# Kernel tuning notes

Hardware: AMD Instinct MI355X
Metric: run time of the kernel (lower is better)

Reference implementation:

```python
import jax, jax.numpy as jnp
import numpy as np
from jax import lax

B, CIN, IMG = 32, 3, 128   # batch, image channels, image size
D, K = 256, 512            # codebook dim, codebook size


def _conv(x, w, stride, pad):
    # PyTorch Conv2d (bias=False), NCHW / OIHW
    return lax.conv_general_dilated(x, w, (stride, stride), ((pad, pad), (pad, pad)),
                                    dimension_numbers=('NCHW', 'OIHW', 'NCHW'))


def _deconv(x, w, b):
    # PyTorch ConvTranspose2d(k=4, s=2, p=1): lhs_dilation=2, pad=k-1-p=2, flipped kernel,
    # weight layout (in, out, kh, kw) -> 'IOHW'
    y = lax.conv_general_dilated(x, jnp.flip(w, (2, 3)), (1, 1), ((2, 2), (2, 2)),
                                 lhs_dilation=(2, 2),
                                 dimension_numbers=('NCHW', 'IOHW', 'NCHW'))
    return y + b[None, :, None, None]


def _res(x, w1, w2):
    # Faithful to the source ResidualBlock: relu1 output is DISCARDED (conv1 applied to x)
    out = _conv(x, w1, 1, 1)      # 3x3, pad 1
    out = jax.nn.relu(out)
    out = _conv(out, w2, 1, 0)    # 1x1, pad 0
    return out + x


def setup_inputs() -> dict:
    key = jax.random.key(0)
    ks = jax.random.split(key, 20)
    s = 0.05
    inp = {
        'x': jax.random.uniform(ks[0], (B, CIN, IMG, IMG), jnp.float32),
        # codebook, init uniform(-1/K, 1/K) as in init_weights
        'embed_w': jax.random.uniform(ks[1], (K, D), jnp.float32, -1.0 / K, 1.0 / K),
        # encoder
        'e_w1': jax.random.normal(ks[2], (D, CIN, 4, 4), jnp.float32) * s,
        'e_w2': jax.random.normal(ks[3], (D, D, 4, 4), jnp.float32) * s,
        'e_r1a': jax.random.normal(ks[4], (D, D, 3, 3), jnp.float32) * s,
        'e_r1b': jax.random.normal(ks[5], (D, D, 1, 1), jnp.float32) * s,
        'e_r2a': jax.random.normal(ks[6], (D, D, 3, 3), jnp.float32) * s,
        'e_r2b': jax.random.normal(ks[7], (D, D, 1, 1), jnp.float32) * s,
        # decoder
        'd_r1a': jax.random.normal(ks[8], (D, D, 3, 3), jnp.float32) * s,
        'd_r1b': jax.random.normal(ks[9], (D, D, 1, 1), jnp.float32) * s,
        'd_r2a': jax.random.normal(ks[10], (D, D, 3, 3), jnp.float32) * s,
        'd_r2b': jax.random.normal(ks[11], (D, D, 1, 1), jnp.float32) * s,
        'dt1_w': jax.random.normal(ks[12], (D, D, 4, 4), jnp.float32) * s,  # (in,out,kh,kw)
        'dt1_b': jnp.zeros((D,), jnp.float32),
        'dt2_w': jax.random.normal(ks[13], (D, CIN, 4, 4), jnp.float32) * s,
        'dt2_b': jnp.zeros((CIN,), jnp.float32),
    }
    return inp


def reference(x, embed_w, e_w1, e_w2, e_r1a, e_r1b, e_r2a, e_r2b,
              d_r1a, d_r1b, d_r2a, d_r2b, dt1_w, dt1_b, dt2_w, dt2_b):
    # ---- encoder (BN layers exist but are never called in the source forward) ----
    h = jax.nn.relu(_conv(x, e_w1, 2, 1))          # (B,D,64,64)
    h = jax.nn.relu(_conv(h, e_w2, 2, 1))          # (B,D,32,32)
    h = _res(h, e_r1a, e_r1b)
    z_e = _res(h, e_r2a, e_r2b)                    # (B,D,H,W)

    # ---- vector quantisation ----
    ze = jnp.transpose(z_e, (0, 2, 3, 1))          # (B,H,W,D)
    # squared L2 distances via expansion (same argmin/values as the broadcast diff tensor)
    d2 = (jnp.sum(ze * ze, -1, keepdims=True)      # (B,H,W,1)
          - 2.0 * jnp.einsum('bhwd,kd->bhwk', ze, embed_w)
          + jnp.sum(embed_w * embed_w, -1))        # (B,H,W,K)
    dist = jnp.sqrt(jnp.maximum(d2, 0.0))          # torch.norm(p=2) before min
    idx = jnp.argmin(dist, axis=-1)                # (B,H,W)
    z_q = embed_w[idx]                             # (B,H,W,D) gather

    # losses: source averages over an extra duplicated K axis, identical to mean over B,H,W
    sg = lax.stop_gradient
    loss1 = jnp.mean(jnp.sum((ze - sg(z_q)) ** 2, -1))   # grads -> encoder
    loss2 = jnp.mean(jnp.sum((sg(ze) - z_q) ** 2, -1))   # grads -> codebook

    # ---- decoder (takes z_q; BN layers never called; relu after deconv1 only) ----
    dq = jnp.transpose(z_q, (0, 3, 1, 2))          # (B,D,H,W)
    dq = _res(dq, d_r1a, d_r1b)
    dq = _res(dq, d_r2a, d_r2b)
    dq = jax.nn.relu(_deconv(dq, dt1_w, dt1_b))    # (B,D,64,64)
    recon = jax.nn.sigmoid(_deconv(dq, dt2_w, dt2_b))  # (B,3,128,128)
    return recon, loss1, loss2
```

## Files before the change

kernel.cpp:

```cpp
#include <hip/hip_runtime.h>


typedef __attribute__((ext_vector_type(8))) short bf16x8;
typedef __attribute__((ext_vector_type(4))) float f32x4;
#define MFMA_B16(a, b, c) __builtin_amdgcn_mfma_f32_16x16x32_bf16(a, b, c, 0, 0, 0)

__device__ inline unsigned short f2b(float f) {
    unsigned int u = __float_as_uint(f);
    unsigned int r = u + 0x7fffu + ((u >> 16) & 1u);
    return (unsigned short)(r >> 16);
}
__device__ inline float b2f(unsigned short u) {
    return __uint_as_float(((unsigned int)u) << 16);
}

struct PermfArgs {
    const float* src[10];
    int kw[10];
    int so[10], si[10], sh[10], sw[10];
    int cum[11];
};

__global__ void prep_all_k(PermfArgs a, unsigned short* __restrict__ dst,
                           const float* __restrict__ dt2_w, unsigned short* __restrict__ wg,
                           const float* __restrict__ embed, unsigned short* __restrict__ embF,
                           const float* __restrict__ e_w1, unsigned short* __restrict__ wgc,
                           float* __restrict__ nrm, float* __restrict__ lacc)
{
    int blkid = blockIdx.x;
    int tid = threadIdx.x;
    if (blkid < 18432) {
        int gid = blkid * 256 + tid;
        if (gid >= a.cum[10]) return;
        int seg = 0;
        while (seg < 9 && gid >= a.cum[seg + 1]) ++seg;
        int l = gid - a.cum[seg];
        int q = l & 31;
        int n = (l >> 5) & 255;
        int rest = l >> 13;
        int cch = rest & 7;
        int khkw = rest >> 3;
        int kh = khkw / a.kw[seg], kw = khkw % a.kw[seg];
        int ci = cch * 32 + q;
        dst[gid] = f2b(a.src[seg][n * a.so[seg] + ci * a.si[seg] + kh * a.sh[seg] + kw * a.sw[seg]]);
        return;
    }
    int blk = blkid - 18432;
    if (blk < 48) {
        int idx = blk * 256 + tid;
        int q = idx & 31;
        int n = (idx >> 5) % 48;
        int cch = idx / (48 * 32);
        int ci = cch * 32 + q;
        int oc = n % 3, khkw = n / 3;
        int kh = khkw >> 2, kw = khkw & 3;
        wg[idx] = f2b(dt2_w[ci * 48 + oc * 16 + kh * 4 + kw]);
    } else if (blk < 560) {
        int idx = (blk - 48) * 256 + tid;
        int q = idx & 31;
        int n = (idx >> 5) & 511;
        int cch = idx >> 14;
        embF[idx] = f2b(embed[n * 256 + cch * 32 + q]);
    } else if (blk < 624) {
        int idx = (blk - 560) * 256 + tid;
        int q = idx & 31;
        int n = (idx >> 5) & 255;
        int kt = idx >> 13;
        int k = kt * 32 + q;
        float v = 0.f;
        if (k < 48) {
            int ci = k >> 4, kh = (k >> 2) & 3, kwv = k & 3;
            v = e_w1[n * 48 + ci * 16 + kh * 4 + kwv];
        }
        wgc[idx] = f2b(v);
    } else if (blk < 752) {
        int row = (blk - 624) * 4 + (tid >> 6);
        int lane = tid & 63;
        float s = 0.f;
        #pragma unroll
        for (int c = 0; c < 256; c += 64) {
            float v = embed[row * 256 + c + lane];
            s += v * v;
        }
        #pragma unroll
        for (int off = 1; off < 64; off <<= 1) s += __shfl_xor(s, off);
        if (lane == 0) nrm[row] = s;
    } else {
        if (tid == 0) lacc[0] = 0.f;
    }
}

__global__ void __launch_bounds__(256, 4)
conv1m_k(const float* __restrict__ x, const unsigned short* __restrict__ wgc,
         unsigned short* __restrict__ out)
{
    int bh = blockIdx.x;
    int b = bh >> 6, oh = bh & 63;
    int tid = threadIdx.x;
    int lane = tid & 63, wv = tid >> 6;
    int m = lane & 15, quad = lane >> 4;
    __shared__ float xrow[3][4][130];
    __shared__ __align__(16) unsigned short imc[64 * 72];
    for (int s = tid; s < 1560; s += 256) {
        int col = s % 130;
        int t = s / 130;
        int r = t & 3;
        int c = t >> 2;
        int ih = 2 * oh - 1 + r, iw = col - 1;
        float v = 0.f;
        if ((unsigned)ih < 128u && (unsigned)iw < 128u)
            v = x[(((b * 3 + c) << 7) + ih) * 128 + iw];
        xrow[c][r][col] = v;
    }
    __syncthreads();
    for (int s = tid; s < 4096; s += 256) {
        int px = s >> 6, k = s & 63;
        float v = 0.f;
        if (k < 48) {
            int ci = k >> 4, kh = (k >> 2) & 3, kw = k & 3;
            v = xrow[ci][kh][2 * px + kw];
        }
        imc[px * 72 + k] = f2b(v);
    }
    __syncthreads();
    f32x4 acc[16];
    f32x4 z = {0.f, 0.f, 0.f, 0.f};
    #pragma unroll
    for (int i = 0; i < 16; ++i) acc[i] = z;
    bf16x8 a0 = *(const bf16x8*)&imc[((wv << 4) + m) * 72 + (quad << 3)];
    bf16x8 a1 = *(const bf16x8*)&imc[((wv << 4) + m) * 72 + 32 + (quad << 3)];
    #pragma unroll
    for (int nt = 0; nt < 16; ++nt) {
        bf16x8 b0 = *(const bf16x8*)&wgc[(nt * 16 + m) * 32 + (quad << 3)];
        bf16x8 b1 = *(const bf16x8*)&wgc[(256 + nt * 16 + m) * 32 + (quad << 3)];
        acc[nt] = MFMA_B16(a0, b0, acc[nt]);
        acc[nt] = MFMA_B16(a1, b1, acc[nt]);
    }
    #pragma unroll
    for (int nt = 0; nt < 16; ++nt)
        #pragma unroll
        for (int r = 0; r < 4; ++r) {
            int px = (wv << 4) + quad * 4 + r;
            out[(((bh << 6) + px) << 8) + nt * 16 + (lane & 15)] = f2b(fmaxf(acc[nt][r], 0.f));
        }
}

__global__ void __launch_bounds__(256, 3)
mconv2_k(const unsigned short* __restrict__ in, const unsigned short* __restrict__ wf,
         unsigned short* __restrict__ out)
{
    int blk = blockIdx.x;
    int bb = blk >> 4, j = blk & 15;
    int lane = threadIdx.x & 63;
    int n0 = (threadIdx.x >> 6) << 6;
    int m = lane & 15, quad = lane >> 4;
    __shared__ __align__(16) unsigned short win[2 * 66 * 132];
    f32x4 acc[2][2][4];
    f32x4 z = {0.f, 0.f, 0.f, 0.f};
    #pragma unroll
    for (int a = 0; a < 2; ++a)
        #pragma unroll
        for (int i = 0; i < 2; ++i)
            #pragma unroll
            for (int t = 0; t < 4; ++t) acc[a][i][t] = z;

    for (int c0 = 0; c0 < 256; c0 += 128) {
        for (int kh = 0; kh < 4; ++kh) {
            __syncthreads();
            for (int s = threadIdx.x; s < 2 * 66 * 16; s += 256) {
                int c16 = s & 15;
                int t2 = s >> 4;
                int col = t2 % 66;
                int rr = t2 / 66;
                int ih = 4 * j - 1 + kh + 2 * rr, iw = col - 1;
                int4 v = make_int4(0, 0, 0, 0);
                if ((unsigned)ih < 64u && (unsigned)iw < 64u)
                    v = *(const int4*)&in[((((bb << 6) + ih) << 6) + iw) * 256 + c0 + (c16 << 3)];
                int cs = (col >> 1) + (col & 1) * 33;
                *(int4*)&win[(rr * 66 + cs) * 132 + (c16 << 3)] = v;
            }
            __syncthreads();
            #pragma unroll
            for (int kw = 0; kw < 4; ++kw) {
                int csoff = (kw >> 1) + (kw & 1) * 33;
                #pragma unroll
                for (int cch = 0; cch < 4; ++cch) {
                    bf16x8 a00 = *(const bf16x8*)&win[(m + csoff) * 132 + (cch << 5) + (quad << 3)];
                    bf16x8 a01 = *(const bf16x8*)&win[(m + 16 + csoff) * 132 + (cch << 5) + (quad << 3)];
                    bf16x8 a10 = *(const bf16x8*)&win[(66 + m + csoff) * 132 + (cch << 5) + (quad << 3)];
                    bf16x8 a11 = *(const bf16x8*)&win[(66 + m + 16 + csoff) * 132 + (cch << 5) + (quad << 3)];
                    int cg = (c0 >> 5) + cch;
                    int wbase = ((((kh << 2) + kw) * 8 + cg) * 256 + n0 + m) * 32 + (quad << 3);
                    bf16x8 b0 = *(const bf16x8*)&wf[wbase];
                    bf16x8 b1 = *(const bf16x8*)&wf[wbase + 16 * 32];
                    bf16x8 b2 = *(const bf16x8*)&wf[wbase + 32 * 32];
                    bf16x8 b3 = *(const bf16x8*)&wf[wbase + 48 * 32];
                    acc[0][0][0] = MFMA_B16(a00, b0, acc[0][0][0]);
                    acc[0][0][1] = MFMA_B16(a00, b1, acc[0][0][1]);
                    acc[0][0][2] = MFMA_B16(a00, b2, acc[0][0][2]);
                    acc[0][0][3] = MFMA_B16(a00, b3, acc[0][0][3]);
                    acc[0][1][0] = MFMA_B16(a01, b0, acc[0][1][0]);
                    acc[0][1][1] = MFMA_B16(a01, b1, acc[0][1][1]);
                    acc[0][1][2] = MFMA_B16(a01, b2, acc[0][1][2]);
                    acc[0][1][3] = MFMA_B16(a01, b3, acc[0][1][3]);
                    acc[1][0][0] = MFMA_B16(a10, b0, acc[1][0][0]);
                    acc[1][0][1] = MFMA_B16(a10, b1, acc[1][0][1]);
                    acc[1][0][2] = MFMA_B16(a10, b2, acc[1][0][2]);
                    acc[1][0][3] = MFMA_B16(a10, b3, acc[1][0][3]);
                    acc[1][1][0] = MFMA_B16(a11, b0, acc[1][1][0]);
                    acc[1][1][1] = MFMA_B16(a11, b1, acc[1][1][1]);
                    acc[1][1][2] = MFMA_B16(a11, b2, acc[1][1][2]);
                    acc[1][1][3] = MFMA_B16(a11, b3, acc[1][1][3]);
                }
            }
        }
    }
    #pragma unroll
    for (int row = 0; row < 2; ++row) {
        int oh = 2 * j + row;
        #pragma unroll
        for (int mt = 0; mt < 2; ++mt)
            #pragma unroll
            for (int nt = 0; nt < 4; ++nt)
                #pragma unroll
                for (int r = 0; r < 4; ++r) {
                    int px = mt * 16 + quad * 4 + r;
                    int col = n0 + nt * 16 + m;
                    out[((((bb << 5) + oh) << 5) + px) * 256 + col] = f2b(fmaxf(acc[row][mt][nt][r], 0.f));
                }
    }
}

__global__ void __launch_bounds__(256, 4)
mres_k(const unsigned short* __restrict__ in, const unsigned short* __restrict__ wf3,
       const unsigned short* __restrict__ wf1, const unsigned short* __restrict__ res,
       unsigned short* __restrict__ outb, float* __restrict__ outf, int f32out)
{
    int blk = blockIdx.x;
    int bb = blk >> 4, j = blk & 15;
    int lane = threadIdx.x & 63;
    int n0 = (threadIdx.x >> 6) << 6;
    int m = lane & 15, quad = lane >> 4;
    __shared__ __align__(16) unsigned short win[4 * 34 * 132];
    f32x4 acc[2][2][4];
    f32x4 z = {0.f, 0.f, 0.f, 0.f};
    #pragma unroll
    for (int a = 0; a < 2; ++a)
        #pragma unroll
        for (int i = 0; i < 2; ++i)
            #pragma unroll
            for (int t = 0; t < 4; ++t) acc[a][i][t] = z;

    for (int c0 = 0; c0 < 256; c0 += 128) {
        __syncthreads();
        for (int s = threadIdx.x; s < 4 * 34 * 16; s += 256) {
            int c16 = s & 15;
            int t2 = s >> 4;
            int col = t2 % 34;
            int rr = t2 / 34;
            int ih = 2 * j - 1 + rr, iw = col - 1;
            int4 v = make_int4(0, 0, 0, 0);
            if ((unsigned)ih < 32u && (unsigned)iw < 32u)
                v = *(const int4*)&in[((((bb << 5) + ih) << 5) + iw) * 256 + c0 + (c16 << 3)];
            *(int4*)&win[(rr * 34 + col) * 132 + (c16 << 3)] = v;
        }
        __syncthreads();
        for (int kh = 0; kh < 3; ++kh) {
            #pragma unroll
            for (int kw = 0; kw < 3; ++kw) {
                #pragma unroll
                for (int cch = 0; cch < 4; ++cch) {
                    const unsigned short* ba = &win[(kh * 34 + m + kw) * 132 + (cch << 5) + (quad << 3)];
                    bf16x8 a00 = *(const bf16x8*)ba;
                    bf16x8 a01 = *(const bf16x8*)(ba + 16 * 132);
                    bf16x8 a10 = *(const bf16x8*)(ba + 34 * 132);
                    bf16x8 a11 = *(const bf16x8*)(ba + 50 * 132);
                    int cg = (c0 >> 5) + cch;
                    int wbase = (((kh * 3 + kw) * 8 + cg) * 256 + n0 + m) * 32 + (quad << 3);
                    bf16x8 b0 = *(const bf16x8*)&wf3[wbase];
                    bf16x8 b1 = *(const bf16x8*)&wf3[wbase + 16 * 32];
                    bf16x8 b2 = *(const bf16x8*)&wf3[wbase + 32 * 32];
                    bf16x8 b3 = *(const bf16x8*)&wf3[wbase + 48 * 32];
                    acc[0][0][0] = MFMA_B16(a00, b0, acc[0][0][0]);
                    acc[0][0][1] = MFMA_B16(a00, b1, acc[0][0][1]);
                    acc[0][0][2] = MFMA_B16(a00, b2, acc[0][0][2]);
                    acc[0][0][3] = MFMA_B16(a00, b3, acc[0][0][3]);
                    acc[0][1][0] = MFMA_B16(a01, b0, acc[0][1][0]);
                    acc[0][1][1] = MFMA_B16(a01, b1, acc[0][1][1]);
                    acc[0][1][2] = MFMA_B16(a01, b2, acc[0][1][2]);
                    acc[0][1][3] = MFMA_B16(a01, b3, acc[0][1][3]);
                    acc[1][0][0] = MFMA_B16(a10, b0, acc[1][0][0]);
                    acc[1][0][1] = MFMA_B16(a10, b1, acc[1][0][1]);
                    acc[1][0][2] = MFMA_B16(a10, b2, acc[1][0][2]);
                    acc[1][0][3] = MFMA_B16(a10, b3, acc[1][0][3]);
                    acc[1][1][0] = MFMA_B16(a11, b0, acc[1][1][0]);
                    acc[1][1][1] = MFMA_B16(a11, b1, acc[1][1][1]);
                    acc[1][1][2] = MFMA_B16(a11, b2, acc[1][1][2]);
                    acc[1][1][3] = MFMA_B16(a11, b3, acc[1][1][3]);
                }
            }
        }
    }

    __syncthreads();
    unsigned short* mid = win;
    #pragma unroll
    for (int row = 0; row < 2; ++row)
        #pragma unroll
        for (int mt = 0; mt < 2; ++mt)
            #pragma unroll
            for (int nt = 0; nt < 4; ++nt)
                #pragma unroll
                for (int r = 0; r < 4; ++r) {
                    int px = row * 32 + mt * 16 + quad * 4 + r;
                    int col = n0 + nt * 16 + m;
                    mid[px * 264 + col] = f2b(fmaxf(acc[row][mt][nt][r], 0.f));
                }
    __syncthreads();

    f32x4 acc2[4][4];
    #pragma unroll
    for (int i = 0; i < 4; ++i)
        #pragma unroll
        for (int t = 0; t < 4; ++t) acc2[i][t] = z;
    #pragma unroll
    for (int cch = 0; cch < 8; ++cch) {
        bf16x8 a0 = *(const bf16x8*)&mid[m * 264 + (cch << 5) + (quad << 3)];
        bf16x8 a1 = *(const bf16x8*)&mid[(m + 16) * 264 + (cch << 5) + (quad << 3)];
        bf16x8 a2 = *(const bf16x8*)&mid[(m + 32) * 264 + (cch << 5) + (quad << 3)];
        bf16x8 a3 = *(const bf16x8*)&mid[(m + 48) * 264 + (cch << 5) + (quad << 3)];
        int wbase = (cch * 256 + n0 + m) * 32 + (quad << 3);
        bf16x8 b0 = *(const bf16x8*)&wf1[wbase];
        bf16x8 b1 = *(const bf16x8*)&wf1[wbase + 16 * 32];
        bf16x8 b2 = *(const bf16x8*)&wf1[wbase + 32 * 32];
        bf16x8 b3 = *(const bf16x8*)&wf1[wbase + 48 * 32];
        acc2[0][0] = MFMA_B16(a0, b0, acc2[0][0]);
        acc2[0][1] = MFMA_B16(a0, b1, acc2[0][1]);
        acc2[0][2] = MFMA_B16(a0, b2, acc2[0][2]);
        acc2[0][3] = MFMA_B16(a0, b3, acc2[0][3]);
        acc2[1][0] = MFMA_B16(a1, b0, acc2[1][0]);
        acc2[1][1] = MFMA_B16(a1, b1, acc2[1][1]);
        acc2[1][2] = MFMA_B16(a1, b2, acc2[1][2]);
        acc2[1][3] = MFMA_B16(a1, b3, acc2[1][3]);
        acc2[2][0] = MFMA_B16(a2, b0, acc2[2][0]);
        acc2[2][1] = MFMA_B16(a2, b1, acc2[2][1]);
        acc2[2][2] = MFMA_B16(a2, b2, acc2[2][2]);
        acc2[2][3] = MFMA_B16(a2, b3, acc2[2][3]);
        acc2[3][0] = MFMA_B16(a3, b0, acc2[3][0]);
        acc2[3][1] = MFMA_B16(a3, b1, acc2[3][1]);
        acc2[3][2] = MFMA_B16(a3, b2, acc2[3][2]);
        acc2[3][3] = MFMA_B16(a3, b3, acc2[3][3]);
    }
    int rowbase = blk << 14;
    #pragma unroll
    for (int mt = 0; mt < 4; ++mt)
        #pragma unroll
        for (int nt = 0; nt < 4; ++nt)
            #pragma unroll
            for (int r = 0; r < 4; ++r) {
                int px = mt * 16 + quad * 4 + r;
                int col = n0 + nt * 16 + m;
                int idx = rowbase + (px << 8) + col;
                float v = acc2[mt][nt][r] + b2f(res[idx]);
                outb[idx] = f2b(v);
                if (f32out) outf[idx] = v;
            }
}

__global__ void __launch_bounds__(256, 4)
mdeconv1_k(const unsigned short* __restrict__ in, const unsigned short* __restrict__ wf,
           const float* __restrict__ bias, unsigned short* __restrict__ out)
{
    int blk = blockIdx.x;
    int bb = blk >> 5;
    int rem = blk & 31;
    int pp = rem >> 4;
    int i = rem & 15;
    int oy_a = pp + 4 * i;
    int p = (oy_a + 1) & 1;
    int r0a = (oy_a + 1 - p) >> 1;
    int rbase = r0a - 1;
    int lane = threadIdx.x & 63;
    int n0 = (threadIdx.x >> 6) << 6;
    int m = lane & 15, quad = lane >> 4;
    __shared__ __align__(16) unsigned short win[2 * 34 * 264];

    auto stage_row = [&](int slot, int r) {
        int ih = rbase + r;
        for (int s = threadIdx.x; s < 34 * 32; s += 256) {
            int c8 = s & 31;
            int col = s >> 5;
            int iw = col - 1;
            int4 v = make_int4(0, 0, 0, 0);
            if ((unsigned)ih < 32u && (unsigned)iw < 32u)
                v = *(const int4*)&in[((((bb << 5) + ih) << 5) + iw) * 256 + (c8 << 3)];
            *(int4*)&win[(slot * 34 + col) * 264 + (c8 << 3)] = v;
        }
    };

    for (int par = 0; par < 2; ++par) {
        f32x4 acc[2][2][4];
        f32x4 z = {0.f, 0.f, 0.f, 0.f};
        #pragma unroll
        for (int a = 0; a < 2; ++a)
            #pragma unroll
            for (int i2 = 0; i2 < 2; ++i2)
                #pragma unroll
                for (int t = 0; t < 4; ++t) acc[a][i2][t] = z;

        __syncthreads();
        stage_row(0, 0);
        if (par == 0) stage_row(1, 1);
        __syncthreads();
        #pragma unroll
        for (int ph = 0; ph < 2; ++ph) {
            int t = 1 - ph;
            int kh = p + 2 * t;
            int slotA = ph;
            int slotB = 1 - ph;
            if (ph == 1) {
                __syncthreads();
                stage_row(0, 2);
                __syncthreads();
            }
            #pragma unroll
            for (int u = 0; u < 2; ++u) {
                int kw = (1 - par) + 2 * u;
                int ixoff = par - u + 1;
                #pragma unroll
                for (int cch = 0; cch < 8; ++cch) {
                    const unsigned short* baA = &win[(slotA * 34 + m + ixoff) * 264 + (cch << 5) + (quad << 3)];
                    const unsigned short* baB = &win[(slotB * 34 + m + ixoff) * 264 + (cch << 5) + (quad << 3)];
                    bf16x8 a00 = *(const bf16x8*)baA;
                    bf16x8 a01 = *(const bf16x8*)(baA + 16 * 264);
                    bf16x8 a10 = *(const bf16x8*)baB;
                    bf16x8 a11 = *(const bf16x8*)(baB + 16 * 264);
                    int wbase = ((((kh << 2) + kw) * 8 + cch) * 256 + n0 + m) * 32 + (quad << 3);
                    bf16x8 b0 = *(const bf16x8*)&wf[wbase];
                    bf16x8 b1 = *(const bf16x8*)&wf[wbase + 16 * 32];
                    bf16x8 b2 = *(const bf16x8*)&wf[wbase + 32 * 32];
                    bf16x8 b3 = *(const bf16x8*)&wf[wbase + 48 * 32];
                    acc[0][0][0] = MFMA_B16(a00, b0, acc[0][0][0]);
                    acc[0][0][1] = MFMA_B16(a00, b1, acc[0][0][1]);
                    acc[0][0][2] = MFMA_B16(a00, b2, acc[0][0][2]);
                    acc[0][0][3] = MFMA_B16(a00, b3, acc[0][0][3]);
                    acc[0][1][0] = MFMA_B16(a01, b0, acc[0][1][0]);
                    acc[0][1][1] = MFMA_B16(a01, b1, acc[0][1][1]);
                    acc[0][1][2] = MFMA_B16(a01, b2, acc[0][1][2]);
                    acc[0][1][3] = MFMA_B16(a01, b3, acc[0][1][3]);
                    acc[1][0][0] = MFMA_B16(a10, b0, acc[1][0][0]);
                    acc[1][0][1] = MFMA_B16(a10, b1, acc[1][0][1]);
                    acc[1][0][2] = MFMA_B16(a10, b2, acc[1][0][2]);
                    acc[1][0][3] = MFMA_B16(a10, b3, acc[1][0][3]);
                    acc[1][1][0] = MFMA_B16(a11, b0, acc[1][1][0]);
                    acc[1][1][1] = MFMA_B16(a11, b1, acc[1][1][1]);
                    acc[1][1][2] = MFMA_B16(a11, b2, acc[1][1][2]);
                    acc[1][1][3] = MFMA_B16(a11, b3, acc[1][1][3]);
                }
            }
        }
        #pragma unroll
        for (int row = 0; row < 2; ++row) {
            int oy = oy_a + 2 * row;
            #pragma unroll
            for (int mt = 0; mt < 2; ++mt)
                #pragma unroll
                for (int nt = 0; nt < 4; ++nt) {
                    int col = n0 + nt * 16 + m;
                    float bs = bias[col];
                    #pragma unroll
                    for (int r = 0; r < 4; ++r) {
                        int ox = 2 * (mt * 16 + quad * 4 + r) + par;
                        float v = fmaxf(acc[row][mt][nt][r] + bs, 0.f);
                        out[((((bb << 6) + oy) << 6) + ox) * 256 + col] = f2b(v);
                    }
                }
        }
    }
}

__global__ void __launch_bounds__(256, 2)
vqm_k(const unsigned short* __restrict__ zeb, const float* __restrict__ zef,
      const unsigned short* __restrict__ embF, const float* __restrict__ embed,
      const float* __restrict__ nrm, unsigned short* __restrict__ zq,
      float* __restrict__ lacc)
{
    int bh = blockIdx.x;
    int tid = threadIdx.x;
    int lane = tid & 63;
    int wv = tid >> 6;
    int m = lane & 15, quad = lane >> 4;
    __shared__ __align__(16) unsigned short win[32 * 264];
    __shared__ float bvv[4][32];
    __shared__ int   bii[4][32];
    __shared__ int   bidx[32];
    int rowbase = bh << 13;
    for (int s = tid; s < 32 * 32; s += 256) {
        int c8 = s & 31, px = s >> 5;
        *(int4*)&win[px * 264 + (c8 << 3)] = *(const int4*)&zeb[rowbase + (px << 8) + (c8 << 3)];
    }
    __syncthreads();

    f32x4 acc[2][8];
    f32x4 z = {0.f, 0.f, 0.f, 0.f};
    #pragma unroll
    for (int i = 0; i < 2; ++i)
        #pragma unroll
        for (int j = 0; j < 8; ++j) acc[i][j] = z;

    #pragma unroll
    for (int cch = 0; cch < 8; ++cch) {
        bf16x8 a0 = *(const bf16x8*)&win[m * 264 + (cch << 5) + (quad << 3)];
        bf16x8 a1 = *(const bf16x8*)&win[(m + 16) * 264 + (cch << 5) + (quad << 3)];
        #pragma unroll
        for (int nt = 0; nt < 8; ++nt) {
            bf16x8 b = *(const bf16x8*)&embF[((cch << 9) + (wv << 7) + (nt << 4) + m) * 32 + (quad << 3)];
            acc[0][nt] = MFMA_B16(a0, b, acc[0][nt]);
            acc[1][nt] = MFMA_B16(a1, b, acc[1][nt]);
        }
    }

    float nv[8];
    #pragma unroll
    for (int nt = 0; nt < 8; ++nt) nv[nt] = nrm[(wv << 7) + (nt << 4) + m];

    #pragma unroll
    for (int mt = 0; mt < 2; ++mt)
        #pragma unroll
        for (int r = 0; r < 4; ++r) {
            float bv = 1e30f;
            int bi = 0x7fffffff;
            #pragma unroll
            for (int nt = 0; nt < 8; ++nt) {
                float d = nv[nt] - 2.f * acc[mt][nt][r];
                int n = (wv << 7) + (nt << 4) + m;
                if (d < bv || (d == bv && n < bi)) { bv = d; bi = n; }
            }
            #pragma unroll
            for (int off = 1; off < 16; off <<= 1) {
                float ov = __shfl_xor(bv, off);
                int oi = __shfl_xor(bi, off);
                if (ov < bv || (ov == bv && oi < bi)) { bv = ov; bi = oi; }
            }
            if (m == 0) {
                int px = mt * 16 + quad * 4 + r;
                bvv[wv][px] = bv;
                bii[wv][px] = bi;
            }
        }
    __syncthreads();
    if (tid < 32) {
        float bv = bvv[0][tid];
        int bi = bii[0][tid];
        #pragma unroll
        for (int w2 = 1; w2 < 4; ++w2) {
            float ov = bvv[w2][tid];
            int oi = bii[w2][tid];
            if (ov < bv || (ov == bv && oi < bi)) { bv = ov; bi = oi; }
        }
        bidx[tid] = bi;
    }
    __syncthreads();

    float lsum = 0.f;
    #pragma unroll
    for (int j = 0; j < 8; ++j) {
        int px = (wv << 3) + j;
        int bi = bidx[px];
        int pix = (bh << 5) + px;
        const float4 e = *(const float4*)&embed[bi * 256 + (lane << 2)];
        const float4 zv = *(const float4*)&zef[(pix << 8) + (lane << 2)];
        ushort4 eq;
        eq.x = f2b(e.x); eq.y = f2b(e.y); eq.z = f2b(e.z); eq.w = f2b(e.w);
        *(ushort4*)&zq[(pix << 8) + (lane << 2)] = eq;
        float dx = zv.x - e.x, dy = zv.y - e.y, dz = zv.z - e.z, dw = zv.w - e.w;
        lsum += dx * dx + dy * dy + dz * dz + dw * dw;
    }
    #pragma unroll
    for (int off = 1; off < 64; off <<= 1) lsum += __shfl_xor(lsum, off);
    if (lane == 0) atomicAdd(lacc, lsum);
}

__global__ void __launch_bounds__(256, 4)
mdec2a_k(const unsigned short* __restrict__ in, const unsigned short* __restrict__ wg,
         float* __restrict__ Y)
{
    int tid = threadIdx.x;
    int lane = tid & 63;
    int wv = tid >> 6;
    int m = lane & 15, quad = lane >> 4;
    __shared__ __align__(16) unsigned short win[64 * 264];
    int pxbase = blockIdx.x << 6;
    for (int s = tid; s < 64 * 32; s += 256) {
        int c8 = s & 31, px = s >> 5;
        *(int4*)&win[px * 264 + (c8 << 3)] = *(const int4*)&in[((pxbase + px) << 8) + (c8 << 3)];
    }
    __syncthreads();
    f32x4 acc[3];
    f32x4 z = {0.f, 0.f, 0.f, 0.f};
    acc[0] = z; acc[1] = z; acc[2] = z;
    #pragma unroll
    for (int cch = 0; cch < 8; ++cch) {
        bf16x8 a = *(const bf16x8*)&win[((wv << 4) + m) * 264 + (cch << 5) + (quad << 3)];
        #pragma unroll
        for (int nt = 0; nt < 3; ++nt) {
            bf16x8 b = *(const bf16x8*)&wg[(cch * 48 + nt * 16 + m) * 32 + (quad << 3)];
            acc[nt] = MFMA_B16(a, b, acc[nt]);
        }
    }
    #pragma unroll
    for (int nt = 0; nt < 3; ++nt)
        #pragma unroll
        for (int r = 0; r < 4; ++r) {
            int px = pxbase + (wv << 4) + quad * 4 + r;
            Y[px * 48 + nt * 16 + m] = acc[nt][r];
        }
}

__global__ void dec2b_k(const float* __restrict__ Y, const float* __restrict__ bias,
                        const float* __restrict__ lacc, float* __restrict__ out)
{
    if (blockIdx.x == 0 && threadIdx.x == 0) {
        float mloss = lacc[0] * (1.0f / 32768.0f);
        out[1572864] = mloss;
        out[1572865] = mloss;
    }
    int idx = blockIdx.x * 256 + threadIdx.x;
    int b = idx >> 14;
    int rem = idx & 16383;
    int oy = rem >> 7;
    int ox = rem & 127;
    int p = (oy + 1) & 1;
    int q = (ox + 1) & 1;
    float acc0 = bias[0], acc1 = bias[1], acc2 = bias[2];
    #pragma unroll
    for (int t = 0; t < 2; ++t) {
        int kh = p + 2 * t;
        int ih = (oy + 1 - kh) >> 1;
        if ((unsigned)ih >= 64u) continue;
        #pragma unroll
        for (int u = 0; u < 2; ++u) {
            int kw = q + 2 * u;
            int iw = (ox + 1 - kw) >> 1;
            if ((unsigned)iw >= 64u) continue;
            int base = ((((b << 6) + ih) << 6) + iw) * 48 + ((kh << 2) + kw) * 3;
            acc0 += Y[base];
            acc1 += Y[base + 1];
            acc2 += Y[base + 2];
        }
    }
    int obase = (b * 3 << 14) + (oy << 7) + ox;
    out[obase]           = 1.f / (1.f + expf(-acc0));
    out[obase + 16384]   = 1.f / (1.f + expf(-acc1));
    out[obase + 32768]   = 1.f / (1.f + expf(-acc2));
}

extern "C" void kernel_launch(void* const* d_in, const int* in_sizes, int n_in,
                              void* d_out, int out_size, void* d_ws, size_t ws_size,
                              hipStream_t stream)
{
    (void)in_sizes; (void)n_in; (void)out_size; (void)ws_size;
    const float* x      = (const float*)d_in[0];
    const float* embed  = (const float*)d_in[1];
    const float* e_w1   = (const float*)d_in[2];
    const float* e_w2   = (const float*)d_in[3];
    const float* e_r1a  = (const float*)d_in[4];
    const float* e_r1b  = (const float*)d_in[5];
    const float* e_r2a  = (const float*)d_in[6];
    const float* e_r2b  = (const float*)d_in[7];
    const float* d_r1a  = (const float*)d_in[8];
    const float* d_r1b  = (const float*)d_in[9];
    const float* d_r2a  = (const float*)d_in[10];
    const float* d_r2b  = (const float*)d_in[11];
    const float* dt1_w  = (const float*)d_in[12];
    const float* dt1_b  = (const float*)d_in[13];
    const float* dt2_w  = (const float*)d_in[14];
    const float* dt2_b  = (const float*)d_in[15];
    float* outp = (float*)d_out;

    char* base = (char*)d_ws;
    size_t off = 0;
    auto alloc = [&](size_t bytes) { char* p = base + off; off += (bytes + 255) & ~size_t(255); return p; };
    unsigned short* A0b = (unsigned short*)alloc(67108864);
    float*          A1f = (float*)alloc(33554432);
    unsigned short* L0  = (unsigned short*)alloc(16777216);
    unsigned short* L1  = (unsigned short*)alloc(16777216);
    unsigned short* Wf  = (unsigned short*)alloc(9437184);
    unsigned short* Wg  = (unsigned short*)alloc(24576);
    unsigned short* EmbF = (unsigned short*)alloc(262144);
    unsigned short* WgC = (unsigned short*)alloc(32768);
    float* Nrm  = (float*)alloc(2048);
    float* Lacc = (float*)alloc(64);
    float* Y = A1f;

    unsigned short* Wf_ew2  = Wf;
    unsigned short* Wf_er1a = Wf + 1048576;
    unsigned short* Wf_er1b = Wf + 1638400;
    unsigned short* Wf_er2a = Wf + 1703936;
    unsigned short* Wf_er2b = Wf + 2293760;
    unsigned short* Wf_dr1a = Wf + 2359296;
    unsigned short* Wf_dr1b = Wf + 2949120;
    unsigned short* Wf_dr2a = Wf + 3014656;
    unsigned short* Wf_dr2b = Wf + 3604480;
    unsigned short* Wf_dt1  = Wf + 3670016;

    PermfArgs pa;
    const float* srcs[10] = {e_w2, e_r1a, e_r1b, e_r2a, e_r2b, d_r1a, d_r1b, d_r2a, d_r2b, dt1_w};
    int kws[10] = {4, 3, 1, 3, 1, 3, 1, 3, 1, 4};
    int sos[10] = {4096, 2304, 256, 2304, 256, 2304, 256, 2304, 256, 16};
    int sis[10] = {16, 9, 1, 9, 1, 9, 1, 9, 1, 4096};
    int shs[10] = {4, 3, 0, 3, 0, 3, 0, 3, 0, 4};
    int sws[10] = {1, 1, 0, 1, 0, 1, 0, 1, 0, 1};
    int cums[11] = {0, 1048576, 1638400, 1703936, 2293760, 2359296,
                    2949120, 3014656, 3604480, 3670016, 4718592};
    for (int k = 0; k < 10; ++k) {
        pa.src[k] = srcs[k]; pa.kw[k] = kws[k]; pa.so[k] = sos[k];
        pa.si[k] = sis[k]; pa.sh[k] = shs[k]; pa.sw[k] = sws[k];
        pa.cum[k] = cums[k];
    }
    pa.cum[10] = cums[10];

    prep_all_k<<<19185, 256, 0, stream>>>(pa, Wf, dt2_w, Wg, embed, EmbF, e_w1, WgC, Nrm, Lacc);

    conv1m_k<<<32 * 64, 256, 0, stream>>>(x, WgC, A0b);
    mconv2_k<<<32 * 16, 256, 0, stream>>>(A0b, Wf_ew2, L1);
    mres_k<<<32 * 16, 256, 0, stream>>>(L1, Wf_er1a, Wf_er1b, L1, L0, nullptr, 0);
    mres_k<<<32 * 16, 256, 0, stream>>>(L0, Wf_er2a, Wf_er2b, L0, L1, A1f, 1);

    vqm_k<<<32 * 32, 256, 0, stream>>>(L1, A1f, EmbF, embed, Nrm, L1, Lacc);

    mres_k<<<32 * 16, 256, 0, stream>>>(L1, Wf_dr1a, Wf_dr1b, L1, L0, nullptr, 0);
    mres_k<<<32 * 16, 256, 0, stream>>>(L0, Wf_dr2a, Wf_dr2b, L0, L1, nullptr, 0);
    mdeconv1_k<<<32 * 32, 256, 0, stream>>>(L1, Wf_dt1, dt1_b, A0b);
    mdec2a_k<<<2048, 256, 0, stream>>>(A0b, Wg, Y);
    dec2b_k<<<2048, 256, 0, stream>>>(Y, dt2_b, Lacc, outp);
}
```

Baseline: 865.2 us.

## Split conv, residual and deconv kernels into smaller tiles for more blocks

The encoder conv2, the residual blocks and deconv1 are re-tiled so each workgroup computes half as many output channels or one output row instead of two. Grid sizes double (or quadruple for deconv1) and per-wave accumulators shrink, which lowers register pressure and allows more waves per CU. The aim is better occupancy and load balance across the many CUs. The cost is more redundant staging of input windows into shared memory and less reuse of each loaded A/B fragment per MFMA.

```diff
diff --git a/kernel.cpp b/kernel.cpp
--- a/kernel.cpp
+++ b/kernel.cpp
@@ -145,24 +145,27 @@
         }
 }
 
-__global__ void __launch_bounds__(256, 3)
+__global__ void __launch_bounds__(256, 4)
 mconv2_k(const unsigned short* __restrict__ in, const unsigned short* __restrict__ wf,
          unsigned short* __restrict__ out)
 {
     int blk = blockIdx.x;
-    int bb = blk >> 4, j = blk & 15;
+    int bb = blk >> 5;
+    int rem = blk & 31;
+    int j = rem >> 1;
+    int nh = rem & 1;
     int lane = threadIdx.x & 63;
-    int n0 = (threadIdx.x >> 6) << 6;
+    int n0 = (nh << 7) + ((threadIdx.x >> 6) << 5);
     int m = lane & 15, quad = lane >> 4;
     __shared__ __align__(16) unsigned short win[2 * 66 * 132];
-    f32x4 acc[2][2][4];
+    f32x4 acc[2][2][2];
     f32x4 z = {0.f, 0.f, 0.f, 0.f};
     #pragma unroll
     for (int a = 0; a < 2; ++a)
         #pragma unroll
         for (int i = 0; i < 2; ++i)
             #pragma unroll
-            for (int t = 0; t < 4; ++t) acc[a][i][t] = z;
+            for (int t = 0; t < 2; ++t) acc[a][i][t] = z;
 
     for (int c0 = 0; c0 < 256; c0 += 128) {
         for (int kh = 0; kh < 4; ++kh) {
@@ -193,24 +196,14 @@
                     int wbase = ((((kh << 2) + kw) * 8 + cg) * 256 + n0 + m) * 32 + (quad << 3);
                     bf16x8 b0 = *(const bf16x8*)&wf[wbase];
                     bf16x8 b1 = *(const bf16x8*)&wf[wbase + 16 * 32];
-                    bf16x8 b2 = *(const bf16x8*)&wf[wbase + 32 * 32];
-                    bf16x8 b3 = *(const bf16x8*)&wf[wbase + 48 * 32];
                     acc[0][0][0] = MFMA_B16(a00, b0, acc[0][0][0]);
                     acc[0][0][1] = MFMA_B16(a00, b1, acc[0][0][1]);
-                    acc[0][0][2] = MFMA_B16(a00, b2, acc[0][0][2]);
-                    acc[0][0][3] = MFMA_B16(a00, b3, acc[0][0][3]);
                     acc[0][1][0] = MFMA_B16(a01, b0, acc[0][1][0]);
                     acc[0][1][1] = MFMA_B16(a01, b1, acc[0][1][1]);
-                    acc[0][1][2] = MFMA_B16(a01, b2, acc[0][1][2]);
-                    acc[0][1][3] = MFMA_B16(a01, b3, acc[0][1][3]);
                     acc[1][0][0] = MFMA_B16(a10, b0, acc[1][0][0]);
                     acc[1][0][1] = MFMA_B16(a10, b1, acc[1][0][1]);
-                    acc[1][0][2] = MFMA_B16(a10, b2, acc[1][0][2]);
-                    acc[1][0][3] = MFMA_B16(a10, b3, acc[1][0][3]);
                     acc[1][1][0] = MFMA_B16(a11, b0, acc[1][1][0]);
                     acc[1][1][1] = MFMA_B16(a11, b1, acc[1][1][1]);
-                    acc[1][1][2] = MFMA_B16(a11, b2, acc[1][1][2]);
-                    acc[1][1][3] = MFMA_B16(a11, b3, acc[1][1][3]);
                 }
             }
         }
@@ -221,7 +214,7 @@
         #pragma unroll
         for (int mt = 0; mt < 2; ++mt)
             #pragma unroll
-            for (int nt = 0; nt < 4; ++nt)
+            for (int nt = 0; nt < 2; ++nt)
                 #pragma unroll
                 for (int r = 0; r < 4; ++r) {
                     int px = mt * 16 + quad * 4 + r;
@@ -237,28 +230,26 @@
        unsigned short* __restrict__ outb, float* __restrict__ outf, int f32out)
 {
     int blk = blockIdx.x;
-    int bb = blk >> 4, j = blk & 15;
+    int bb = blk >> 5, oh = blk & 31;
     int lane = threadIdx.x & 63;
     int n0 = (threadIdx.x >> 6) << 6;
     int m = lane & 15, quad = lane >> 4;
-    __shared__ __align__(16) unsigned short win[4 * 34 * 132];
-    f32x4 acc[2][2][4];
+    __shared__ __align__(16) unsigned short win[3 * 34 * 132];
+    f32x4 acc[2][4];
     f32x4 z = {0.f, 0.f, 0.f, 0.f};
     #pragma unroll
-    for (int a = 0; a < 2; ++a)
-        #pragma unroll
-        for (int i = 0; i < 2; ++i)
-            #pragma unroll
-            for (int t = 0; t < 4; ++t) acc[a][i][t] = z;
+    for (int i = 0; i < 2; ++i)
+        #pragma unroll
+        for (int t = 0; t < 4; ++t) acc[i][t] = z;
 
     for (int c0 = 0; c0 < 256; c0 += 128) {
         __syncthreads();
-        for (int s = threadIdx.x; s < 4 * 34 * 16; s += 256) {
+        for (int s = threadIdx.x; s < 3 * 34 * 16; s += 256) {
             int c16 = s & 15;
             int t2 = s >> 4;
             int col = t2 % 34;
             int rr = t2 / 34;
-            int ih = 2 * j - 1 + rr, iw = col - 1;
+            int ih = oh - 1 + rr, iw = col - 1;
             int4 v = make_int4(0, 0, 0, 0);
             if ((unsigned)ih < 32u && (unsigned)iw < 32u)
                 v = *(const int4*)&in[((((bb << 5) + ih) << 5) + iw) * 256 + c0 + (c16 << 3)];
@@ -271,32 +262,22 @@
                 #pragma unroll
                 for (int cch = 0; cch < 4; ++cch) {
                     const unsigned short* ba = &win[(kh * 34 + m + kw) * 132 + (cch << 5) + (quad << 3)];
-                    bf16x8 a00 = *(const bf16x8*)ba;
-                    bf16x8 a01 = *(const bf16x8*)(ba + 16 * 132);
-                    bf16x8 a10 = *(const bf16x8*)(ba + 34 * 132);
-                    bf16x8 a11 = *(const bf16x8*)(ba + 50 * 132);
+                    bf16x8 a0 = *(const bf16x8*)ba;
+                    bf16x8 a1 = *(const bf16x8*)(ba + 16 * 132);
                     int cg = (c0 >> 5) + cch;
                     int wbase = (((kh * 3 + kw) * 8 + cg) * 256 + n0 + m) * 32 + (quad << 3);
                     bf16x8 b0 = *(const bf16x8*)&wf3[wbase];
                     bf16x8 b1 = *(const bf16x8*)&wf3[wbase + 16 * 32];
                     bf16x8 b2 = *(const bf16x8*)&wf3[wbase + 32 * 32];
                     bf16x8 b3 = *(const bf16x8*)&wf3[wbase + 48 * 32];
-                    acc[0][0][0] = MFMA_B16(a00, b0, acc[0][0][0]);
-                    acc[0][0][1] = MFMA_B16(a00, b1, acc[0][0][1]);
-                    acc[0][0][2] = MFMA_B16(a00, b2, acc[0][0][2]);
-                    acc[0][0][3] = MFMA_B16(a00, b3, acc[0][0][3]);
-                    acc[0][1][0] = MFMA_B16(a01, b0, acc[0][1][0]);
-                    acc[0][1][1] = MFMA_B16(a01, b1, acc[0][1][1]);
-                    acc[0][1][2] = MFMA_B16(a01, b2, acc[0][1][2]);
-                    acc[0][1][3] = MFMA_B16(a01, b3, acc[0][1][3]);
-                    acc[1][0][0] = MFMA_B16(a10, b0, acc[1][0][0]);
-                    acc[1][0][1] = MFMA_B16(a10, b1, acc[1][0][1]);
-                    acc[1][0][2] = MFMA_B16(a10, b2, acc[1][0][2]);
-                    acc[1][0][3] = MFMA_B16(a10, b3, acc[1][0][3]);
-                    acc[1][1][0] = MFMA_B16(a11, b0, acc[1][1][0]);
-                    acc[1][1][1] = MFMA_B16(a11, b1, acc[1][1][1]);
-                    acc[1][1][2] = MFMA_B16(a11, b2, acc[1][1][2]);
-                    acc[1][1][3] = MFMA_B16(a11, b3, acc[1][1][3]);
+                    acc[0][0] = MFMA_B16(a0, b0, acc[0][0]);
+                    acc[0][1] = MFMA_B16(a0, b1, acc[0][1]);
+                    acc[0][2] = MFMA_B16(a0, b2, acc[0][2]);
+                    acc[0][3] = MFMA_B16(a0, b3, acc[0][3]);
+                    acc[1][0] = MFMA_B16(a1, b0, acc[1][0]);
+                    acc[1][1] = MFMA_B16(a1, b1, acc[1][1]);
+                    acc[1][2] = MFMA_B16(a1, b2, acc[1][2]);
+                    acc[1][3] = MFMA_B16(a1, b3, acc[1][3]);
                 }
             }
         }
@@ -305,30 +286,26 @@
     __syncthreads();
     unsigned short* mid = win;
     #pragma unroll
-    for (int row = 0; row < 2; ++row)
-        #pragma unroll
-        for (int mt = 0; mt < 2; ++mt)
-            #pragma unroll
-            for (int nt = 0; nt < 4; ++nt)
-                #pragma unroll
-                for (int r = 0; r < 4; ++r) {
-                    int px = row * 32 + mt * 16 + quad * 4 + r;
-                    int col = n0 + nt * 16 + m;
-                    mid[px * 264 + col] = f2b(fmaxf(acc[row][mt][nt][r], 0.f));
-                }
-    __syncthreads();
-
-    f32x4 acc2[4][4];
-    #pragma unroll
-    for (int i = 0; i < 4; ++i)
+    for (int mt = 0; mt < 2; ++mt)
+        #pragma unroll
+        for (int nt = 0; nt < 4; ++nt)
+            #pragma unroll
+            for (int r = 0; r < 4; ++r) {
+                int px = mt * 16 + quad * 4 + r;
+                int col = n0 + nt * 16 + m;
+                mid[px * 264 + col] = f2b(fmaxf(acc[mt][nt][r], 0.f));
+            }
+    __syncthreads();
+
+    f32x4 acc2[2][4];
+    #pragma unroll
+    for (int i = 0; i < 2; ++i)
         #pragma unroll
         for (int t = 0; t < 4; ++t) acc2[i][t] = z;
     #pragma unroll
     for (int cch = 0; cch < 8; ++cch) {
         bf16x8 a0 = *(const bf16x8*)&mid[m * 264 + (cch << 5) + (quad << 3)];
         bf16x8 a1 = *(const bf16x8*)&mid[(m + 16) * 264 + (cch << 5) + (quad << 3)];
-        bf16x8 a2 = *(const bf16x8*)&mid[(m + 32) * 264 + (cch << 5) + (quad << 3)];
-        bf16x8 a3 = *(const bf16x8*)&mid[(m + 48) * 264 + (cch << 5) + (quad << 3)];
         int wbase = (cch * 256 + n0 + m) * 32 + (quad << 3);
         bf16x8 b0 = *(const bf16x8*)&wf1[wbase];
         bf16x8 b1 = *(const bf16x8*)&wf1[wbase + 16 * 32];
@@ -342,18 +319,10 @@
         acc2[1][1] = MFMA_B16(a1, b1, acc2[1][1]);
         acc2[1][2] = MFMA_B16(a1, b2, acc2[1][2]);
         acc2[1][3] = MFMA_B16(a1, b3, acc2[1][3]);
-        acc2[2][0] = MFMA_B16(a2, b0, acc2[2][0]);
-        acc2[2][1] = MFMA_B16(a2, b1, acc2[2][1]);
-        acc2[2][2] = MFMA_B16(a2, b2, acc2[2][2]);
-        acc2[2][3] = MFMA_B16(a2, b3, acc2[2][3]);
-        acc2[3][0] = MFMA_B16(a3, b0, acc2[3][0]);
-        acc2[3][1] = MFMA_B16(a3, b1, acc2[3][1]);
-        acc2[3][2] = MFMA_B16(a3, b2, acc2[3][2]);
-        acc2[3][3] = MFMA_B16(a3, b3, acc2[3][3]);
-    }
-    int rowbase = blk << 14;
-    #pragma unroll
-    for (int mt = 0; mt < 4; ++mt)
+    }
+    int rowbase = blk << 13;
+    #pragma unroll
+    for (int mt = 0; mt < 2; ++mt)
         #pragma unroll
         for (int nt = 0; nt < 4; ++nt)
             #pragma unroll
@@ -372,110 +341,92 @@
            const float* __restrict__ bias, unsigned short* __restrict__ out)
 {
     int blk = blockIdx.x;
-    int bb = blk >> 5;
-    int rem = blk & 31;
-    int pp = rem >> 4;
-    int i = rem & 15;
+    int bb = blk >> 7;
+    int rem = blk & 127;
+    int par = rem & 1;
+    int nh = (rem >> 1) & 1;
+    int r2 = rem >> 2;
+    int pp = r2 >> 4;
+    int i = r2 & 15;
     int oy_a = pp + 4 * i;
     int p = (oy_a + 1) & 1;
     int r0a = (oy_a + 1 - p) >> 1;
     int rbase = r0a - 1;
     int lane = threadIdx.x & 63;
-    int n0 = (threadIdx.x >> 6) << 6;
+    int n0 = (nh << 7) + ((threadIdx.x >> 6) << 5);
     int m = lane & 15, quad = lane >> 4;
-    __shared__ __align__(16) unsigned short win[2 * 34 * 264];
-
-    auto stage_row = [&](int slot, int r) {
-        int ih = rbase + r;
-        for (int s = threadIdx.x; s < 34 * 32; s += 256) {
-            int c8 = s & 31;
-            int col = s >> 5;
-            int iw = col - 1;
+    __shared__ __align__(16) unsigned short win[3 * 34 * 132];
+
+    f32x4 acc[2][2][2];
+    f32x4 z = {0.f, 0.f, 0.f, 0.f};
+    #pragma unroll
+    for (int a = 0; a < 2; ++a)
+        #pragma unroll
+        for (int i2 = 0; i2 < 2; ++i2)
+            #pragma unroll
+            for (int t = 0; t < 2; ++t) acc[a][i2][t] = z;
+
+    for (int c0 = 0; c0 < 256; c0 += 128) {
+        __syncthreads();
+        for (int s = threadIdx.x; s < 3 * 34 * 16; s += 256) {
+            int c16 = s & 15;
+            int t2 = s >> 4;
+            int col = t2 % 34;
+            int rr = t2 / 34;
+            int ih = rbase + rr, iw = col - 1;
             int4 v = make_int4(0, 0, 0, 0);
             if ((unsigned)ih < 32u && (unsigned)iw < 32u)
-                v = *(const int4*)&in[((((bb << 5) + ih) << 5) + iw) * 256 + (c8 << 3)];
-            *(int4*)&win[(slot * 34 + col) * 264 + (c8 << 3)] = v;
-        }
-    };
-
-    for (int par = 0; par < 2; ++par) {
-        f32x4 acc[2][2][4];
-        f32x4 z = {0.f, 0.f, 0.f, 0.f};
-        #pragma unroll
-        for (int a = 0; a < 2; ++a)
-            #pragma unroll
-            for (int i2 = 0; i2 < 2; ++i2)
-                #pragma unroll
-                for (int t = 0; t < 4; ++t) acc[a][i2][t] = z;
-
+                v = *(const int4*)&in[((((bb << 5) + ih) << 5) + iw) * 256 + c0 + (c16 << 3)];
+            *(int4*)&win[(rr * 34 + col) * 132 + (c16 << 3)] = v;
+        }
         __syncthreads();
-        stage_row(0, 0);
-        if (par == 0) stage_row(1, 1);
-        __syncthreads();
-        #pragma unroll
-        for (int ph = 0; ph < 2; ++ph) {
-            int t = 1 - ph;
+        #pragma unroll
+        for (int t = 0; t < 2; ++t) {
             int kh = p + 2 * t;
-            int slotA = ph;
-            int slotB = 1 - ph;
-            if (ph == 1) {
-                __syncthreads();
-                stage_row(0, 2);
-                __syncthreads();
-            }
             #pragma unroll
             for (int u = 0; u < 2; ++u) {
                 int kw = (1 - par) + 2 * u;
                 int ixoff = par - u + 1;
                 #pragma unroll
-                for (int cch = 0; cch < 8; ++cch) {
-                    const unsigned short* baA = &win[(slotA * 34 + m + ixoff) * 264 + (cch << 5) + (quad << 3)];
-                    const unsigned short* baB = &win[(slotB * 34 + m + ixoff) * 264 + (cch << 5) + (quad << 3)];
+                for (int cch = 0; cch < 4; ++cch) {
+                    const unsigned short* baA = &win[((1 - t) * 34 + m + ixoff) * 132 + (cch << 5) + (quad << 3)];
+                    const unsigned short* baB = &win[((2 - t) * 34 + m + ixoff) * 132 + (cch << 5) + (quad << 3)];
                     bf16x8 a00 = *(const bf16x8*)baA;
-                    bf16x8 a01 = *(const bf16x8*)(baA + 16 * 264);
+                    bf16x8 a01 = *(const bf16x8*)(baA + 16 * 132);
                     bf16x8 a10 = *(const bf16x8*)baB;
-                    bf16x8 a11 = *(const bf16x8*)(baB + 16 * 264);
-                    int wbase = ((((kh << 2) + kw) * 8 + cch) * 256 + n0 + m) * 32 + (quad << 3);
+                    bf16x8 a11 = *(const bf16x8*)(baB + 16 * 132);
+                    int cg = (c0 >> 5) + cch;
+                    int wbase = ((((kh << 2) + kw) * 8 + cg) * 256 + n0 + m) * 32 + (quad << 3);
                     bf16x8 b0 = *(const bf16x8*)&wf[wbase];
                     bf16x8 b1 = *(const bf16x8*)&wf[wbase + 16 * 32];
-                    bf16x8 b2 = *(const bf16x8*)&wf[wbase + 32 * 32];
-                    bf16x8 b3 = *(const bf16x8*)&wf[wbase + 48 * 32];
                     acc[0][0][0] = MFMA_B16(a00, b0, acc[0][0][0]);
                     acc[0][0][1] = MFMA_B16(a00, b1, acc[0][0][1]);
-                    acc[0][0][2] = MFMA_B16(a00, b2, acc[0][0][2]);
-                    acc[0][0][3] = MFMA_B16(a00, b3, acc[0][0][3]);
                     acc[0][1][0] = MFMA_B16(a01, b0, acc[0][1][0]);
                     acc[0][1][1] = MFMA_B16(a01, b1, acc[0][1][1]);
-                    acc[0][1][2] = MFMA_B16(a01, b2, acc[0][1][2]);
-                    acc[0][1][3] = MFMA_B16(a01, b3, acc[0][1][3]);
                     acc[1][0][0] = MFMA_B16(a10, b0, acc[1][0][0]);
                     acc[1][0][1] = MFMA_B16(a10, b1, acc[1][0][1]);
-                    acc[1][0][2] = MFMA_B16(a10, b2, acc[1][0][2]);
-                    acc[1][0][3] = MFMA_B16(a10, b3, acc[1][0][3]);
                     acc[1][1][0] = MFMA_B16(a11, b0, acc[1][1][0]);
                     acc[1][1][1] = MFMA_B16(a11, b1, acc[1][1][1]);
-                    acc[1][1][2] = MFMA_B16(a11, b2, acc[1][1][2]);
-                    acc[1][1][3] = MFMA_B16(a11, b3, acc[1][1][3]);
                 }
             }
         }
-        #pragma unroll
-        for (int row = 0; row < 2; ++row) {
-            int oy = oy_a + 2 * row;
-            #pragma unroll
-            for (int mt = 0; mt < 2; ++mt)
+    }
+    #pragma unroll
+    for (int row = 0; row < 2; ++row) {
+        int oy = oy_a + 2 * row;
+        #pragma unroll
+        for (int mt = 0; mt < 2; ++mt)
+            #pragma unroll
+            for (int nt = 0; nt < 2; ++nt) {
+                int col = n0 + nt * 16 + m;
+                float bs = bias[col];
                 #pragma unroll
-                for (int nt = 0; nt < 4; ++nt) {
-                    int col = n0 + nt * 16 + m;
-                    float bs = bias[col];
-                    #pragma unroll
-                    for (int r = 0; r < 4; ++r) {
-                        int ox = 2 * (mt * 16 + quad * 4 + r) + par;
-                        float v = fmaxf(acc[row][mt][nt][r] + bs, 0.f);
-                        out[((((bb << 6) + oy) << 6) + ox) * 256 + col] = f2b(v);
-                    }
+                for (int r = 0; r < 4; ++r) {
+                    int ox = 2 * (mt * 16 + quad * 4 + r) + par;
+                    float v = fmaxf(acc[row][mt][nt][r] + bs, 0.f);
+                    out[((((bb << 6) + oy) << 6) + ox) * 256 + col] = f2b(v);
                 }
-        }
+            }
     }
 }
 
@@ -723,15 +674,15 @@
     prep_all_k<<<19185, 256, 0, stream>>>(pa, Wf, dt2_w, Wg, embed, EmbF, e_w1, WgC, Nrm, Lacc);
 
     conv1m_k<<<32 * 64, 256, 0, stream>>>(x, WgC, A0b);
-    mconv2_k<<<32 * 16, 256, 0, stream>>>(A0b, Wf_ew2, L1);
-    mres_k<<<32 * 16, 256, 0, stream>>>(L1, Wf_er1a, Wf_er1b, L1, L0, nullptr, 0);
-    mres_k<<<32 * 16, 256, 0, stream>>>(L0, Wf_er2a, Wf_er2b, L0, L1, A1f, 1);
+    mconv2_k<<<32 * 32, 256, 0, stream>>>(A0b, Wf_ew2, L1);
+    mres_k<<<32 * 32, 256, 0, stream>>>(L1, Wf_er1a, Wf_er1b, L1, L0, nullptr, 0);
+    mres_k<<<32 * 32, 256, 0, stream>>>(L0, Wf_er2a, Wf_er2b, L0, L1, A1f, 1);
 
     vqm_k<<<32 * 32, 256, 0, stream>>>(L1, A1f, EmbF, embed, Nrm, L1, Lacc);
 
-    mres_k<<<32 * 16, 256, 0, stream>>>(L1, Wf_dr1a, Wf_dr1b, L1, L0, nullptr, 0);
-    mres_k<<<32 * 16, 256, 0, stream>>>(L0, Wf_dr2a, Wf_dr2b, L0, L1, nullptr, 0);
-    mdeconv1_k<<<32 * 32, 256, 0, stream>>>(L1, Wf_dt1, dt1_b, A0b);
+    mres_k<<<32 * 32, 256, 0, stream>>>(L1, Wf_dr1a, Wf_dr1b, L1, L0, nullptr, 0);
+    mres_k<<<32 * 32, 256, 0, stream>>>(L0, Wf_dr2a, Wf_dr2b, L0, L1, nullptr, 0);
+    mdeconv1_k<<<32 * 128, 256, 0, stream>>>(L1, Wf_dt1, dt1_b, A0b);
     mdec2a_k<<<2048, 256, 0, stream>>>(A0b, Wg, Y);
     dec2b_k<<<2048, 256, 0, stream>>>(Y, dt2_b, Lacc, outp);
 }
```

Measured after the change: 880.4 us. About the same (+1.8%).
